# Performance work log

Measured on AMD Instinct MI355X. Metric: run time of the kernel, lower is better.

## Reference

```python
import jax, jax.numpy as jnp
import numpy as np

B, L, T, LM, DFF, D, H = 8, 256, 2048, 4096, 1024, 84, 4
HD = D // H  # 21
NCLS = 265


def _ln(x, s, b):
    m = x.mean(-1, keepdims=True)
    v = ((x - m) ** 2).mean(-1, keepdims=True)
    return (x - m) * jax.lax.rsqrt(v + 1e-5) * s + b


def _fourier(xyz, gB):
    # PositionEmbeddingCoordsSine(d_pos=10, pos_type='fourier'): xyz @ B * 2pi -> [sin, cos]
    proj = (2.0 * jnp.pi) * jnp.einsum('bnc,cd->bnd', xyz, gB)  # [B,N,5]
    return jnp.concatenate([jnp.sin(proj), jnp.cos(proj)], axis=-1)  # [B,N,10]


def setup_inputs() -> dict:
    key = jax.random.key(0)
    ks = jax.random.split(key, 20)
    def nrm(k, shape, scale):
        return jax.random.normal(k, shape, jnp.float32) * scale
    coords = jax.random.uniform(ks[0], (B, L, 6), jnp.float32)
    cls = jax.random.randint(ks[1], (B, L), 0, NCLS).astype(jnp.float32)
    vision_features = jnp.concatenate([coords, cls[..., None]], axis=-1)  # [B,L,7]
    FIN = D * L + LM  # 25600
    inp = {
        'grd_tokens': nrm(ks[2], (T, LM), 1.0),
        'vision_features': vision_features,
        'token_batch_idx': jax.random.randint(ks[3], (T,), 0, B),
        'gauss_B': nrm(ks[4], (3, 5), 1.0),
        'class_emb': nrm(ks[5], (NCLS, 64), 0.02),
        'w_in': nrm(ks[6], (2, D, 3 * D), D ** -0.5),
        'b_in': jnp.zeros((2, 3 * D), jnp.float32),
        'w_out': nrm(ks[7], (2, D, D), D ** -0.5),
        'b_out': jnp.zeros((2, D), jnp.float32),
        'ln1_s': jnp.ones((2, D), jnp.float32), 'ln1_b': jnp.zeros((2, D), jnp.float32),
        'w_ff1': nrm(ks[8], (2, D, DFF), D ** -0.5), 'b_ff1': jnp.zeros((2, DFF), jnp.float32),
        'w_ff2': nrm(ks[9], (2, DFF, D), DFF ** -0.5), 'b_ff2': jnp.zeros((2, D), jnp.float32),
        'ln2_s': jnp.ones((2, D), jnp.float32), 'ln2_b': jnp.zeros((2, D), jnp.float32),
        'w0': nrm(ks[10], (FIN, DFF), FIN ** -0.5), 'b0': jnp.zeros((DFF,), jnp.float32),
        'w1': nrm(ks[11], (DFF, DFF), DFF ** -0.5), 'b1': jnp.zeros((DFF,), jnp.float32),
        'w2': nrm(ks[12], (DFF, DFF), DFF ** -0.5), 'b2': jnp.zeros((DFF,), jnp.float32),
        'w3': nrm(ks[13], (DFF, DFF), DFF ** -0.5), 'b3': jnp.zeros((DFF,), jnp.float32),
        'w4': nrm(ks[14], (DFF, 6), DFF ** -0.5), 'b4': jnp.zeros((6,), jnp.float32),
    }
    return inp


def reference(grd_tokens, vision_features, token_batch_idx, gauss_B, class_emb,
              w_in, b_in, w_out, b_out, ln1_s, ln1_b, w_ff1, b_ff1, w_ff2, b_ff2,
              ln2_s, ln2_b, w0, b0, w1, b1, w2, b2, w3, b3, w4, b4):
    pe_min = _fourier(vision_features[:, :, 0:3], gauss_B)  # [B,L,10]
    pe_max = _fourier(vision_features[:, :, 3:6], gauss_B)  # [B,L,10]
    cls = vision_features[:, :, -1].astype(jnp.int32)
    src = jnp.concatenate([pe_min, pe_max, class_emb[cls]], axis=-1)  # [B,L,84]
    pad = jnp.all(vision_features == 0, axis=-1)  # [B,L]
    neg = jnp.where(pad, -1e9, 0.0)[:, None, None, :]  # [B,1,1,L] key-padding bias
    # 2-layer post-norm transformer encoder (DETR-style, pos=None, dropout=0)
    for l in range(2):
        qkv = src @ w_in[l] + b_in[l]
        q, k, v = jnp.split(qkv, 3, axis=-1)
        q = q.reshape(B, L, H, HD)
        k = k.reshape(B, L, H, HD)
        v = v.reshape(B, L, H, HD)
        scores = jnp.einsum('blhd,bmhd->bhlm', q, k) / jnp.sqrt(jnp.float32(HD)) + neg
        attn = jax.nn.softmax(scores, axis=-1)
        o = jnp.einsum('bhlm,bmhd->blhd', attn, v).reshape(B, L, D)
        src = _ln(src + o @ w_out[l] + b_out[l], ln1_s[l], ln1_b[l])
        ff = jax.nn.relu(src @ w_ff1[l] + b_ff1[l]) @ w_ff2[l] + b_ff2[l]
        src = _ln(src + ff, ln2_s[l], ln2_b[l])
    vision_flat = src.reshape(B, L * D)  # flattened encoder output per sample [B, 21504]
    # batched version of the ragged python loop: gather per-token vision feat + concat lm feat
    feat = jnp.concatenate([vision_flat[token_batch_idx], grd_tokens], axis=-1)  # [T, 25600]
    h = jax.nn.relu(feat @ w0 + b0)
    h = jax.nn.relu(h @ w1 + b1)
    h = jax.nn.relu(h @ w2 + b2)
    h = jax.nn.relu(h @ w3 + b3)
    return h @ w4 + b4  # [T, 6]
```

## Files before the change

### kernel.cpp

```cpp
#include <hip/hip_runtime.h>
#include <hip/hip_bf16.h>

#define B_ 8
#define L_ 256
#define T_ 2048
#define LM_ 4096
#define DFF_ 1024
#define D_ 84
#define H_ 4
#define HD_ 21
#define BL_ (B_*L_)
#define VISF_ (L_*D_)
#define VKS 168
#define VCHUNK (VISF_/VKS)
#define AKS 8
#define AKEYS (L_/AKS)

typedef __attribute__((ext_vector_type(8))) short bf16x8;
typedef __attribute__((ext_vector_type(4))) float f32x4;

typedef const __attribute__((address_space(1))) int* gas_p;
typedef __attribute__((address_space(3))) int* las_p;
__device__ __forceinline__ void gld_lds16(const void* g, void* l) {
    __builtin_amdgcn_global_load_lds((gas_p)g, (las_p)l, 16, 0, 0);
}

struct bh4 { __hip_bfloat16 x, y, z, w; };



__device__ __forceinline__ void dev_wT_pack(const float* __restrict__ W,
        __hip_bfloat16* __restrict__ Wp, int K, int N, int kb, int nb, int tid,
        float (*t)[33])
{
    int tx = tid & 31, ty = tid >> 5;
    #pragma unroll
    for (int i = 0; i < 4; ++i)
        t[ty + i*8][tx] = W[(size_t)(kb + ty + i*8)*N + nb + tx];
    __syncthreads();
    int KG = K >> 3;
    #pragma unroll
    for (int i = 0; i < 4; ++i) {
        int n = nb + ty + i*8, k = kb + tx;
        Wp[((size_t)(n>>4)*KG + (k>>3))*128 + (n&15)*8 + (k&7)] = __float2bfloat16(t[tx][ty + i*8]);
    }
}

__device__ __forceinline__ void dev_wTp_pack(const float* __restrict__ W,
        __hip_bfloat16* __restrict__ Wp, int K, int N, int KP, int kb, int nb, int tid,
        float (*t)[33])
{
    int tx = tid & 31, ty = tid >> 5;
    #pragma unroll
    for (int i = 0; i < 4; ++i) {
        int k = kb + ty + i*8, n = nb + tx;
        t[ty + i*8][tx] = (k < K && n < N) ? W[(size_t)k*N + n] : 0.0f;
    }
    __syncthreads();
    int KG = KP >> 3;
    #pragma unroll
    for (int i = 0; i < 4; ++i) {
        int n = nb + ty + i*8, k = kb + tx;
        Wp[((size_t)(n>>4)*KG + (k>>3))*128 + (n&15)*8 + (k&7)] = __float2bfloat16(t[tx][ty + i*8]);
    }
}

__device__ __forceinline__ void dev_wTp_row(const float* __restrict__ W,
        __hip_bfloat16* __restrict__ WT, int K, int N, int KP, int kb, int nb, int tid,
        float (*t)[33])
{
    int tx = tid & 31, ty = tid >> 5;
    #pragma unroll
    for (int i = 0; i < 4; ++i) {
        int k = kb + ty + i*8, n = nb + tx;
        t[ty + i*8][tx] = (k < K && n < N) ? W[(size_t)k*N + n] : 0.0f;
    }
    __syncthreads();
    #pragma unroll
    for (int i = 0; i < 4; ++i)
        WT[(size_t)(nb + ty + i*8)*KP + kb + tx] = __float2bfloat16(t[tx][ty + i*8]);
}

__device__ __forceinline__ void dev_f2b_pack(const float* __restrict__ in,
        __hip_bfloat16* __restrict__ out, int i)
{
    int row = i >> 9, kc = i & 511;
    const float4* p = reinterpret_cast<const float4*>(in + (size_t)row*4096 + kc*8);
    float4 v0 = p[0], v1 = p[1];
    bh4 a = { __float2bfloat16(v0.x), __float2bfloat16(v0.y),
              __float2bfloat16(v0.z), __float2bfloat16(v0.w) };
    bh4 b = { __float2bfloat16(v1.x), __float2bfloat16(v1.y),
              __float2bfloat16(v1.z), __float2bfloat16(v1.w) };
    __hip_bfloat16* o = out + ((size_t)(row>>4)*512 + kc)*128 + (row&15)*8;
    reinterpret_cast<bh4*>(o)[0] = a;
    reinterpret_cast<bh4*>(o)[1] = b;
}

__device__ __forceinline__ void dev_build_src(const float* __restrict__ vf,
        const float* __restrict__ gB, const float* __restrict__ cemb,
        float* __restrict__ src, float* __restrict__ neg, int row)
{
    float v[7];
    bool allz = true;
    #pragma unroll
    for (int c = 0; c < 7; ++c) { v[c] = vf[row*7 + c]; allz = allz && (v[c] == 0.0f); }
    neg[row] = allz ? -1e9f : 0.0f;
    float* s = src + (size_t)row * D_;
    const float TWO_PI = 6.28318530717958647692f;
    #pragma unroll
    for (int d = 0; d < 5; ++d) {
        float pmin = TWO_PI * (v[0]*gB[d] + v[1]*gB[5+d] + v[2]*gB[10+d]);
        float pmax = TWO_PI * (v[3]*gB[d] + v[4]*gB[5+d] + v[5]*gB[10+d]);
        s[d]      = sinf(pmin);  s[5+d]  = cosf(pmin);
        s[10+d]   = sinf(pmax);  s[15+d] = cosf(pmax);
    }
    int cls = (int)v[6];
    const float4* ce = reinterpret_cast<const float4*>(cemb + (size_t)cls*64);
    float4* so = reinterpret_cast<float4*>(s + 20);
    #pragma unroll
    for (int i = 0; i < 16; ++i) so[i] = ce[i];
}

__global__ __launch_bounds__(256) void k_pack_all(
        const float* __restrict__ grd, const float* __restrict__ w0,
        const float* __restrict__ w1, const float* __restrict__ w2,
        const float* __restrict__ w3, const float* __restrict__ w_ff1,
        const float* __restrict__ w_ff2,
        const float* __restrict__ vf, const float* __restrict__ gB,
        const float* __restrict__ cemb,
        __hip_bfloat16* __restrict__ grdb, __hip_bfloat16* __restrict__ w0t,
        __hip_bfloat16* __restrict__ w1t, __hip_bfloat16* __restrict__ w2t,
        __hip_bfloat16* __restrict__ w3t, __hip_bfloat16* __restrict__ wff1t,
        __hip_bfloat16* __restrict__ wff2t,
        float* __restrict__ src, float* __restrict__ neg)
{
    __shared__ float t[32][33];
    int blk = blockIdx.x, tid = threadIdx.x;
    if (blk < 4096) {
        dev_wT_pack(w0 + (size_t)VISF_*DFF_, w0t, LM_, DFF_,
                    (blk & 127)*32, (blk >> 7)*32, tid, t);
    } else if (blk < 5120) {
        int u = blk - 4096;
        dev_wT_pack(w1, w1t, DFF_, DFF_, (u & 31)*32, (u >> 5)*32, tid, t);
    } else if (blk < 6144) {
        int u = blk - 5120;
        dev_wT_pack(w2, w2t, DFF_, DFF_, (u & 31)*32, (u >> 5)*32, tid, t);
    } else if (blk < 7168) {
        int u = blk - 6144;
        dev_wT_pack(w3, w3t, DFF_, DFF_, (u & 31)*32, (u >> 5)*32, tid, t);
    } else if (blk < 7424) {
        int u = blk - 7168;
        int l = u >> 7; u &= 127;
        dev_wTp_pack(w_ff1 + (size_t)l*D_*DFF_, wff1t + (size_t)l*1024*128,
                     D_, DFF_, 128, (u & 3)*32, (u >> 2)*32, tid, t);
    } else if (blk < 7616) {
        int u = blk - 7424;
        int l = u / 96; u -= l*96;
        dev_wTp_row(w_ff2 + (size_t)l*DFF_*D_, wff2t + (size_t)l*96*1024,
                    DFF_, D_, 1024, (u % 32)*32, (u / 32)*32, tid, t);
    } else if (blk < 11712) {
        dev_f2b_pack(grd, grdb, (blk - 7616)*256 + tid);
    } else {
        dev_build_src(vf, gB, cemb, src, neg, (blk - 11712)*256 + tid);
    }
}

__global__ __launch_bounds__(256) void k_qkv8(const float* __restrict__ src,
        const float* __restrict__ w_in, const float* __restrict__ b_in,
        float* __restrict__ qkv, int lay)
{
    __shared__ float s8[8][D_];
    int r0 = blockIdx.x * 8, tid = threadIdx.x;
    for (int idx = tid; idx < 8*D_; idx += 256) {
        int r = idx / D_, d = idx - r*D_;
        s8[r][d] = src[(size_t)(r0+r)*D_ + d];
    }
    __syncthreads();
    if (tid < 3*D_) {
        const float* w = w_in + (size_t)lay*D_*3*D_ + tid;
        float acc[8] = {};
        for (int d = 0; d < D_; ++d) {
            float wv = w[(size_t)d*3*D_];
            #pragma unroll
            for (int r = 0; r < 8; ++r) acc[r] = fmaf(s8[r][d], wv, acc[r]);
        }
        float bv = b_in[lay*3*D_ + tid];
        #pragma unroll
        for (int r = 0; r < 8; ++r) qkv[(size_t)(r0+r)*(3*D_) + tid] = acc[r] + bv;
    }
}

__global__ __launch_bounds__(256) void k_attn_part(const float* __restrict__ qkv,
        const float* __restrict__ neg, float* __restrict__ part)
{
    __shared__ float ks_[AKEYS*HD_], vs_[AKEYS*HD_], ns[AKEYS];
    int bh = blockIdx.x;
    int b = bh >> 2, h = bh & 3;
    int sp = blockIdx.y;
    int tid = threadIdx.x;
    int k0 = sp * AKEYS;
    for (int idx = tid; idx < AKEYS*HD_; idx += 256) {
        int l = idx / HD_, d = idx - l*HD_;
        size_t base = ((size_t)(b*L_ + k0 + l))*(3*D_) + h*HD_ + d;
        ks_[idx] = qkv[base + D_];
        vs_[idx] = qkv[base + 2*D_];
    }
    if (tid < AKEYS) ns[tid] = neg[b*L_ + k0 + tid];
    __syncthreads();
    float q[HD_];
    {
        size_t base = ((size_t)(b*L_ + tid))*(3*D_) + h*HD_;
        #pragma unroll
        for (int d = 0; d < HD_; ++d) q[d] = qkv[base + d];
    }
    const float scale = 0.21821789023599239f;
    float m_run = -INFINITY, l_run = 0.0f;
    float o[HD_];
    #pragma unroll
    for (int d = 0; d < HD_; ++d) o[d] = 0.0f;
    for (int m = 0; m < AKEYS; ++m) {
        const float* krow = &ks_[m*HD_];
        float sdot = 0.0f;
        #pragma unroll
        for (int d = 0; d < HD_; ++d) sdot = fmaf(q[d], krow[d], sdot);
        float sc = sdot * scale + ns[m];
        float nm = fmaxf(m_run, sc);
        float c = __expf(m_run - nm);
        float p = __expf(sc - nm);
        l_run = l_run * c + p;
        const float* vrow = &vs_[m*HD_];
        #pragma unroll
        for (int d = 0; d < HD_; ++d) o[d] = fmaf(p, vrow[d], o[d]*c);
        m_run = nm;
    }
    float* po = part + (((size_t)bh*AKS + sp)*L_ + tid)*24;
    #pragma unroll
    for (int d = 0; d < HD_; ++d) po[d] = o[d];
    po[21] = m_run;
    po[22] = l_run;
}

__global__ __launch_bounds__(128) void k_oproj_ln(const float* __restrict__ part,
        const float* __restrict__ w_out, const float* __restrict__ b_out,
        const float* __restrict__ ln_s, const float* __restrict__ ln_b,
        float* __restrict__ src, __hip_bfloat16* __restrict__ srcb, int lay)
{
    __shared__ float os[D_];
    __shared__ float r1[128], r2[128];
    int row = blockIdx.x, tid = threadIdx.x;
    int b = row >> 8, q = row & 255;
    if (tid < D_) {
        int h = tid / 21, d = tid - h*21;
        const float* pb = part + (((size_t)(b*H_ + h)*AKS)*L_ + q)*24;
        float m_tot = -INFINITY;
        #pragma unroll
        for (int sp = 0; sp < AKS; ++sp)
            m_tot = fmaxf(m_tot, pb[(size_t)sp*L_*24 + 21]);
        float l_tot = 0.0f, ov = 0.0f;
        #pragma unroll
        for (int sp = 0; sp < AKS; ++sp) {
            const float* pp = pb + (size_t)sp*L_*24;
            float e = __expf(pp[21] - m_tot);
            l_tot = fmaf(pp[22], e, l_tot);
            ov = fmaf(pp[d], e, ov);
        }
        os[tid] = ov / l_tot;
    }
    __syncthreads();
    float y = 0.0f;
    if (tid < D_) {
        const float* w = w_out + (size_t)lay*D_*D_ + tid;
        float acc = b_out[lay*D_ + tid];
        for (int d = 0; d < D_; ++d) acc = fmaf(os[d], w[(size_t)d*D_], acc);
        y = src[(size_t)row*D_ + tid] + acc;
    }
    r1[tid] = (tid < D_) ? y : 0.0f;
    r2[tid] = (tid < D_) ? y*y : 0.0f;
    __syncthreads();
    for (int s = 64; s > 0; s >>= 1) {
        if (tid < s) { r1[tid] += r1[tid+s]; r2[tid] += r2[tid+s]; }
        __syncthreads();
    }
    float mean = r1[0] * (1.0f/D_);
    float var  = r2[0] * (1.0f/D_) - mean*mean;
    float rstd = rsqrtf(var + 1e-5f);
    float out = 0.0f;
    if (tid < D_) {
        out = (y - mean)*rstd*ln_s[lay*D_+tid] + ln_b[lay*D_+tid];
        src[(size_t)row*D_ + tid] = out;
    }
    __hip_bfloat16 val = (tid < D_) ? __float2bfloat16(out) : __float2bfloat16(0.0f);
    srcb[((size_t)(row>>4)*16 + (tid>>3))*128 + (row&15)*8 + (tid&7)] = val;
}

__global__ __launch_bounds__(256) void k_ff2_mfma(
        const __hip_bfloat16* __restrict__ hb,
        const __hip_bfloat16* __restrict__ wt,
        float* __restrict__ part)
{
    __shared__ __align__(16) __hip_bfloat16 sA[2][4096];
    __shared__ __align__(16) __hip_bfloat16 sB[2][6144];
    int tid = threadIdx.x;
    int bm = blockIdx.x * 64, sp = blockIdx.y;
    int wave = tid >> 6, lane = tid & 63;
    int wr = wave >> 1, wc = wave & 1;
    int l15 = lane & 15, l4 = lane >> 4;
    f32x4 acc[2][3] = {};

    const int row0 = bm + (tid & 63);
    const int kb = tid >> 6;
    const __hip_bfloat16* Ap0 = hb + (((size_t)(row0 >> 4)*128) + sp*16 + kb)*128 + (row0 & 15)*8;
    const __hip_bfloat16* Ap1 = Ap0 + 512;
    const int b_i0 = tid,       b_kb0 = b_i0/96, b_n0 = b_i0%96;
    const int b_i1 = tid + 256, b_kb1 = b_i1/96, b_n1 = b_i1%96;
    const int b_i2 = tid + 512, b_kb2 = b_i2/96, b_n2 = b_i2%96;
    const __hip_bfloat16* Bp0 = wt + (size_t)b_n0*1024 + sp*128 + b_kb0*8;
    const __hip_bfloat16* Bp1 = wt + (size_t)b_n1*1024 + sp*128 + b_kb1*8;
    const __hip_bfloat16* Bp2 = wt + (size_t)b_n2*1024 + sp*128 + b_kb2*8;

    gld_lds16(Ap0, (char*)&sA[0][0] + tid*16);
    gld_lds16(Ap1, (char*)&sA[0][0] + (tid+256)*16);
    gld_lds16(Bp0, (char*)&sB[0][0] + b_i0*16);
    gld_lds16(Bp1, (char*)&sB[0][0] + b_i1*16);
    gld_lds16(Bp2, (char*)&sB[0][0] + b_i2*16);
    #pragma unroll
    for (int t = 0; t < 2; ++t) {
        __syncthreads();
        if (t == 0) {
            gld_lds16(Ap0 + 1024, (char*)&sA[1][0] + tid*16);
            gld_lds16(Ap1 + 1024, (char*)&sA[1][0] + (tid+256)*16);
            gld_lds16(Bp0 + 64, (char*)&sB[1][0] + b_i0*16);
            gld_lds16(Bp1 + 64, (char*)&sB[1][0] + b_i1*16);
            gld_lds16(Bp2 + 64, (char*)&sB[1][0] + b_i2*16);
        }
        const __hip_bfloat16* sa = &sA[t][0];
        const __hip_bfloat16* sb = &sB[t][0];
        #pragma unroll
        for (int ks = 0; ks < 2; ++ks) {
            bf16x8 af[2], bfr[3];
            #pragma unroll
            for (int mi = 0; mi < 2; ++mi)
                af[mi] = *reinterpret_cast<const bf16x8*>(
                    &sa[(size_t)((ks*4 + l4)*64 + wr*32 + mi*16 + l15) * 8]);
            #pragma unroll
            for (int ni = 0; ni < 3; ++ni)
                bfr[ni] = *reinterpret_cast<const bf16x8*>(
                    &sb[(size_t)((ks*4 + l4)*96 + wc*48 + ni*16 + l15) * 8]);
            #pragma unroll
            for (int mi = 0; mi < 2; ++mi)
                #pragma unroll
                for (int ni = 0; ni < 3; ++ni)
                    acc[mi][ni] = __builtin_amdgcn_mfma_f32_16x16x32_bf16(
                        af[mi], bfr[ni], acc[mi][ni], 0, 0, 0);
        }
    }
    float* po = part + (size_t)sp*(2048*96);
    #pragma unroll
    for (int mi = 0; mi < 2; ++mi)
        #pragma unroll
        for (int reg = 0; reg < 4; ++reg) {
            int row = bm + wr*32 + mi*16 + l4*4 + reg;
            #pragma unroll
            for (int ni = 0; ni < 3; ++ni) {
                int col = wc*48 + ni*16 + l15;
                po[(size_t)row*96 + col] = acc[mi][ni][reg];
            }
        }
}

__global__ __launch_bounds__(128) void k_ff2ln_red(const float* __restrict__ part,
        const float* __restrict__ b_ff2, const float* __restrict__ ln_s,
        const float* __restrict__ ln_b, float* __restrict__ src, int lay)
{
    __shared__ float r1[128], r2[128];
    int row = blockIdx.x, tid = threadIdx.x;
    float y = 0.0f;
    if (tid < D_) {
        #pragma unroll
        for (int sp = 0; sp < 8; ++sp)
            y += part[(size_t)sp*(2048*96) + (size_t)row*96 + tid];
        y += b_ff2[lay*D_ + tid] + src[(size_t)row*D_ + tid];
    }
    r1[tid] = (tid < D_) ? y : 0.0f;
    r2[tid] = (tid < D_) ? y*y : 0.0f;
    __syncthreads();
    for (int s = 64; s > 0; s >>= 1) {
        if (tid < s) { r1[tid] += r1[tid+s]; r2[tid] += r2[tid+s]; }
        __syncthreads();
    }
    float mean = r1[0] * (1.0f/D_);
    float var  = r2[0] * (1.0f/D_) - mean*mean;
    float rstd = rsqrtf(var + 1e-5f);
    if (tid < D_)
        src[(size_t)row*D_ + tid] = (y - mean)*rstd*ln_s[lay*D_+tid] + ln_b[lay*D_+tid];
}

__global__ __launch_bounds__(256) void k_vis_gemm(const float* __restrict__ src,
        const float* __restrict__ w0, float* __restrict__ partials)
{
    __shared__ float vf[8][VCHUNK];
    __shared__ float red[8][256][4];
    int nt = blockIdx.x, sp = blockIdx.y, tid = threadIdx.x;
    int k0 = sp * VCHUNK;
    for (int idx = tid; idx < 8*VCHUNK; idx += 256) {
        int r = idx >> 7, c = idx & 127;
        vf[r][c] = src[(size_t)r*VISF_ + k0 + c];
    }
    __syncthreads();
    int ng = tid & 31;
    int kh = tid >> 5;
    const float* wp = w0 + (size_t)(k0 + kh*16)*DFF_ + nt*128 + ng*4;
    float acc[8][4] = {};
    #pragma unroll 4
    for (int kk = 0; kk < 16; ++kk) {
        float4 w = *reinterpret_cast<const float4*>(wp + (size_t)kk*DFF_);
        #pragma unroll
        for (int m = 0; m < 8; ++m) {
            float sv = vf[m][kh*16 + kk];
            acc[m][0] = fmaf(sv, w.x, acc[m][0]);
            acc[m][1] = fmaf(sv, w.y, acc[m][1]);
            acc[m][2] = fmaf(sv, w.z, acc[m][2]);
            acc[m][3] = fmaf(sv, w.w, acc[m][3]);
        }
    }
    #pragma unroll
    for (int m = 0; m < 8; ++m)
        *reinterpret_cast<float4*>(&red[m][tid][0]) =
            make_float4(acc[m][0], acc[m][1], acc[m][2], acc[m][3]);
    __syncthreads();
    int m2 = tid >> 5, ng2 = tid & 31;
    float4 s = *reinterpret_cast<const float4*>(&red[m2][ng2][0]);
    #pragma unroll
    for (int j = 1; j < 8; ++j) {
        float4 v = *reinterpret_cast<const float4*>(&red[m2][j*32 + ng2][0]);
        s.x += v.x; s.y += v.y; s.z += v.z; s.w += v.w;
    }
    *reinterpret_cast<float4*>(
        &partials[(size_t)sp*8192 + m2*1024 + nt*128 + ng2*4]) = s;
}

__global__ __launch_bounds__(256) void k_vis_red(const float* __restrict__ partials,
        float* __restrict__ vis)
{
    int o = blockIdx.x*256 + threadIdx.x;
    float s = 0.0f;
    for (int sp = 0; sp < VKS; ++sp) s += partials[(size_t)sp*8192 + o];
    vis[o] = s;
}

template<bool ADD_VIS, int K>
__global__ __launch_bounds__(256) void mfma_gemm(
        const __hip_bfloat16* __restrict__ Ap,
        const __hip_bfloat16* __restrict__ Bp,
        const float* __restrict__ bias,
        const float* __restrict__ vis,
        const int* __restrict__ bidx,
        __hip_bfloat16* __restrict__ Cp)
{
    constexpr int KG = K >> 3;
    constexpr int NG = 128;
    __shared__ __align__(16) __hip_bfloat16 cst[64*128];
    int tid = threadIdx.x, wave = tid >> 6, lane = tid & 63;
    int wr = wave >> 1, wc = wave & 1;
    int l15 = lane & 15, l4 = lane >> 4;
    int bm = blockIdx.x * 64, bn = blockIdx.y * 128;
    const __hip_bfloat16* Aw = Ap + ((size_t)((bm >> 4) + wr*2) * KG) * 128 + lane*8;
    const __hip_bfloat16* Bw = Bp + ((size_t)((bn >> 4) + wc*4) * KG) * 128 + lane*8;
    f32x4 acc[2][4] = {};

    #pragma unroll 4
    for (int kg = 0; kg < KG; kg += 4) {
        bf16x8 a[2], b[4];
        #pragma unroll
        for (int mi = 0; mi < 2; ++mi)
            a[mi] = *reinterpret_cast<const bf16x8*>(Aw + ((size_t)mi*KG + kg)*128);
        #pragma unroll
        for (int ni = 0; ni < 4; ++ni)
            b[ni] = *reinterpret_cast<const bf16x8*>(Bw + ((size_t)ni*KG + kg)*128);
        #pragma unroll
        for (int mi = 0; mi < 2; ++mi)
            #pragma unroll
            for (int ni = 0; ni < 4; ++ni)
                acc[mi][ni] = __builtin_amdgcn_mfma_f32_16x16x32_bf16(
                    a[mi], b[ni], acc[mi][ni], 0, 0, 0);
    }

    #pragma unroll
    for (int mi = 0; mi < 2; ++mi) {
        int mg = wr*2 + mi;
        #pragma unroll
        for (int ni = 0; ni < 4; ++ni) {
            int cg = wc*8 + ni*2 + (l15 >> 3);
            int c  = l15 & 7;
            int col = bn + cg*8 + c;
            float bv = bias[col];
            #pragma unroll
            for (int reg = 0; reg < 4; ++reg) {
                int r = l4*4 + reg;
                float v = acc[mi][ni][reg] + bv;
                if (ADD_VIS) v += vis[(size_t)bidx[bm + mg*16 + r]*1024 + col];
                v = fmaxf(v, 0.0f);
                cst[((mg*16 + cg)*16 + r)*8 + c] = __float2bfloat16(v);
            }
        }
    }
    __syncthreads();
    #pragma unroll
    for (int ch = tid; ch < 1024; ch += 256) {
        int mgcg = ch >> 4, r = ch & 15;
        int mg = mgcg >> 4, cg = mgcg & 15;
        size_t go = ((size_t)((bm >> 4) + mg) * NG + (bn >> 3) + cg) * 128 + r*8;
        *reinterpret_cast<bf16x8*>(Cp + go) =
            *reinterpret_cast<const bf16x8*>(cst + (size_t)ch*8);
    }
}

__global__ __launch_bounds__(64) void k_final(const __hip_bfloat16* __restrict__ hp,
        const float* __restrict__ w4, const float* __restrict__ b4, float* __restrict__ out)
{
    int t = blockIdx.x, lane = threadIdx.x;
    int mg = t >> 4, r = t & 15;
    float acc[6] = {};
    #pragma unroll
    for (int it = 0; it < 2; ++it) {
        int kg = lane + it*64;
        bf16x8 h = *reinterpret_cast<const bf16x8*>(hp + ((size_t)mg*128 + kg)*128 + r*8);
        #pragma unroll
        for (int j = 0; j < 8; ++j) {
            unsigned short us = (unsigned short)h[j];
            float hv = __uint_as_float((unsigned)us << 16);
            int k = kg*8 + j;
            #pragma unroll
            for (int c = 0; c < 6; ++c) acc[c] = fmaf(hv, w4[k*6 + c], acc[c]);
        }
    }
    #pragma unroll
    for (int j = 0; j < 6; ++j)
        #pragma unroll
        for (int s = 32; s > 0; s >>= 1) acc[j] += __shfl_down(acc[j], s);
    if (lane == 0) {
        #pragma unroll
        for (int j = 0; j < 6; ++j) out[(size_t)t*6 + j] = acc[j] + b4[j];
    }
}

extern "C" void kernel_launch(void* const* d_in, const int* in_sizes, int n_in,
                              void* d_out, int out_size, void* d_ws, size_t ws_size,
                              hipStream_t stream)
{
    const float* grd   = (const float*)d_in[0];
    const float* vfeat = (const float*)d_in[1];
    const int*   tbi   = (const int*)  d_in[2];
    const float* gB    = (const float*)d_in[3];
    const float* cemb  = (const float*)d_in[4];
    const float* w_in  = (const float*)d_in[5];
    const float* b_in  = (const float*)d_in[6];
    const float* w_out = (const float*)d_in[7];
    const float* b_out = (const float*)d_in[8];
    const float* ln1_s = (const float*)d_in[9];
    const float* ln1_b = (const float*)d_in[10];
    const float* w_ff1 = (const float*)d_in[11];
    const float* b_ff1 = (const float*)d_in[12];
    const float* w_ff2 = (const float*)d_in[13];
    const float* b_ff2 = (const float*)d_in[14];
    const float* ln2_s = (const float*)d_in[15];
    const float* ln2_b = (const float*)d_in[16];
    const float* w0    = (const float*)d_in[17];
    const float* b0    = (const float*)d_in[18];
    const float* w1    = (const float*)d_in[19];
    const float* b1    = (const float*)d_in[20];
    const float* w2    = (const float*)d_in[21];
    const float* b2    = (const float*)d_in[22];
    const float* w3    = (const float*)d_in[23];
    const float* b3    = (const float*)d_in[24];
    const float* w4    = (const float*)d_in[25];
    const float* b4    = (const float*)d_in[26];

    float* ws = (float*)d_ws;
    float* src    = ws;
    float* neg    = src    + 172032;
    float* qkv    = neg    + 2048;
    float* vparts = qkv    + 516096;
    float* visp   = vparts + 1376256;
    float* ffpart = visp   + 8192;
    float* fend   = ffpart + 1572864;
    __hip_bfloat16* grdb  = (__hip_bfloat16*)fend;
    __hip_bfloat16* w0t   = grdb  + 8388608;
    __hip_bfloat16* w1t   = w0t   + 4194304;
    __hip_bfloat16* w2t   = w1t   + 1048576;
    __hip_bfloat16* w3t   = w2t   + 1048576;
    __hip_bfloat16* hab   = w3t   + 1048576;
    __hip_bfloat16* hbb   = hab   + 2097152;
    __hip_bfloat16* srcb  = hbb   + 2097152;
    __hip_bfloat16* wff1t = srcb  + 262144;
    __hip_bfloat16* wff2t = wff1t + 262144;
    __hip_bfloat16* ffh   = hab;

    k_pack_all<<<11720, 256, 0, stream>>>(grd, w0, w1, w2, w3, w_ff1, w_ff2,
        vfeat, gB, cemb, grdb, w0t, w1t, w2t, w3t, wff1t, wff2t, src, neg);

    for (int lay = 0; lay < 2; ++lay) {
        k_qkv8     <<<BL_/8, 256, 0, stream>>>(src, w_in, b_in, qkv, lay);
        k_attn_part<<<dim3(B_*H_, AKS), 256, 0, stream>>>(qkv, neg, ffpart);
        k_oproj_ln <<<BL_, 128, 0, stream>>>(ffpart, w_out, b_out, ln1_s, ln1_b, src, srcb, lay);
        mfma_gemm<false, 128><<<dim3(32, 8), 256, 0, stream>>>(
            srcb, wff1t + (size_t)lay*1024*128, b_ff1 + lay*DFF_, nullptr, nullptr, ffh);
        k_ff2_mfma<<<dim3(32, 8), 256, 0, stream>>>(
            ffh, wff2t + (size_t)lay*96*1024, ffpart);
        k_ff2ln_red<<<BL_, 128, 0, stream>>>(ffpart, b_ff2, ln2_s, ln2_b, src, lay);
    }

    k_vis_gemm<<<dim3(8, VKS), 256, 0, stream>>>(src, w0, vparts);
    k_vis_red<<<32, 256, 0, stream>>>(vparts, visp);

    dim3 mg(T_/64, DFF_/128);
    mfma_gemm<true,  LM_ ><<<mg, 256, 0, stream>>>(grdb, w0t, b0, visp, tbi, hab);
    mfma_gemm<false, DFF_><<<mg, 256, 0, stream>>>(hab,  w1t, b1, nullptr, nullptr, hbb);
    mfma_gemm<false, DFF_><<<mg, 256, 0, stream>>>(hbb,  w2t, b2, nullptr, nullptr, hab);
    mfma_gemm<false, DFF_><<<mg, 256, 0, stream>>>(hab,  w3t, b3, nullptr, nullptr, hbb);

    k_final<<<T_, 64, 0, stream>>>(hbb, w4, b4, (float*)d_out);
}
```

Before: 240.6 us.

## Fuse QKV projection into attention kernel and read packed ff2 weights directly

```diff
diff --git a/kernel.cpp b/kernel.cpp
--- a/kernel.cpp
+++ b/kernel.cpp
@@ -19,14 +19,7 @@
 typedef __attribute__((ext_vector_type(8))) short bf16x8;
 typedef __attribute__((ext_vector_type(4))) float f32x4;
 
-typedef const __attribute__((address_space(1))) int* gas_p;
-typedef __attribute__((address_space(3))) int* las_p;
-__device__ __forceinline__ void gld_lds16(const void* g, void* l) {
-    __builtin_amdgcn_global_load_lds((gas_p)g, (las_p)l, 16, 0, 0);
-}
-
 struct bh4 { __hip_bfloat16 x, y, z, w; };
-
 
 
 __device__ __forceinline__ void dev_wT_pack(const float* __restrict__ W,
@@ -63,22 +56,6 @@
         int n = nb + ty + i*8, k = kb + tx;
         Wp[((size_t)(n>>4)*KG + (k>>3))*128 + (n&15)*8 + (k&7)] = __float2bfloat16(t[tx][ty + i*8]);
     }
-}
-
-__device__ __forceinline__ void dev_wTp_row(const float* __restrict__ W,
-        __hip_bfloat16* __restrict__ WT, int K, int N, int KP, int kb, int nb, int tid,
-        float (*t)[33])
-{
-    int tx = tid & 31, ty = tid >> 5;
-    #pragma unroll
-    for (int i = 0; i < 4; ++i) {
-        int k = kb + ty + i*8, n = nb + tx;
-        t[ty + i*8][tx] = (k < K && n < N) ? W[(size_t)k*N + n] : 0.0f;
-    }
-    __syncthreads();
-    #pragma unroll
-    for (int i = 0; i < 4; ++i)
-        WT[(size_t)(nb + ty + i*8)*KP + kb + tx] = __float2bfloat16(t[tx][ty + i*8]);
 }
 
 __device__ __forceinline__ void dev_f2b_pack(const float* __restrict__ in,
@@ -156,8 +133,8 @@
     } else if (blk < 7616) {
         int u = blk - 7424;
         int l = u / 96; u -= l*96;
-        dev_wTp_row(w_ff2 + (size_t)l*DFF_*D_, wff2t + (size_t)l*96*1024,
-                    DFF_, D_, 1024, (u % 32)*32, (u / 32)*32, tid, t);
+        dev_wTp_pack(w_ff2 + (size_t)l*DFF_*D_, wff2t + (size_t)l*98304,
+                     DFF_, D_, DFF_, (u % 32)*32, (u / 32)*32, tid, t);
     } else if (blk < 11712) {
         dev_f2b_pack(grd, grdb, (blk - 7616)*256 + tid);
     } else {
@@ -165,53 +142,50 @@
     }
 }
 
-__global__ __launch_bounds__(256) void k_qkv8(const float* __restrict__ src,
+__global__ __launch_bounds__(256) void k_attn_fused(const float* __restrict__ src,
         const float* __restrict__ w_in, const float* __restrict__ b_in,
-        float* __restrict__ qkv, int lay)
-{
-    __shared__ float s8[8][D_];
-    int r0 = blockIdx.x * 8, tid = threadIdx.x;
-    for (int idx = tid; idx < 8*D_; idx += 256) {
-        int r = idx / D_, d = idx - r*D_;
-        s8[r][d] = src[(size_t)(r0+r)*D_ + d];
-    }
-    __syncthreads();
-    if (tid < 3*D_) {
-        const float* w = w_in + (size_t)lay*D_*3*D_ + tid;
-        float acc[8] = {};
-        for (int d = 0; d < D_; ++d) {
-            float wv = w[(size_t)d*3*D_];
-            #pragma unroll
-            for (int r = 0; r < 8; ++r) acc[r] = fmaf(s8[r][d], wv, acc[r]);
+        const float* __restrict__ neg, float* __restrict__ part, int lay)
+{
+    __shared__ float ksrc[AKEYS][D_];
+    __shared__ float wq[D_][HD_], wk[D_][HD_], wv[D_][HD_];
+    __shared__ float ks_[AKEYS][HD_], vs_[AKEYS][HD_], ns[AKEYS];
+    int bh = blockIdx.x, b = bh >> 2, h = bh & 3;
+    int sp = blockIdx.y, tid = threadIdx.x;
+    int k0 = sp * AKEYS;
+    const float* wbase = w_in + (size_t)lay*D_*(3*D_);
+    for (int i = tid; i < D_*HD_; i += 256) {
+        int j = i / HD_, d = i - j*HD_;
+        const float* wr = wbase + (size_t)j*(3*D_) + h*HD_ + d;
+        wq[j][d] = wr[0];
+        wk[j][d] = wr[D_];
+        wv[j][d] = wr[2*D_];
+    }
+    for (int i = tid; i < AKEYS*D_; i += 256) {
+        int r = i / D_, c = i - r*D_;
+        ksrc[r][c] = src[(size_t)(b*L_ + k0 + r)*D_ + c];
+    }
+    if (tid < AKEYS) ns[tid] = neg[b*L_ + k0 + tid];
+    __syncthreads();
+    const float* bb = b_in + lay*(3*D_);
+    for (int i = tid; i < AKEYS*HD_; i += 256) {
+        int r = i / HD_, d = i - r*HD_;
+        float ak = bb[D_ + h*HD_ + d], av = bb[2*D_ + h*HD_ + d];
+        for (int j = 0; j < D_; ++j) {
+            float s = ksrc[r][j];
+            ak = fmaf(s, wk[j][d], ak);
+            av = fmaf(s, wv[j][d], av);
         }
-        float bv = b_in[lay*3*D_ + tid];
-        #pragma unroll
-        for (int r = 0; r < 8; ++r) qkv[(size_t)(r0+r)*(3*D_) + tid] = acc[r] + bv;
-    }
-}
-
-__global__ __launch_bounds__(256) void k_attn_part(const float* __restrict__ qkv,
-        const float* __restrict__ neg, float* __restrict__ part)
-{
-    __shared__ float ks_[AKEYS*HD_], vs_[AKEYS*HD_], ns[AKEYS];
-    int bh = blockIdx.x;
-    int b = bh >> 2, h = bh & 3;
-    int sp = blockIdx.y;
-    int tid = threadIdx.x;
-    int k0 = sp * AKEYS;
-    for (int idx = tid; idx < AKEYS*HD_; idx += 256) {
-        int l = idx / HD_, d = idx - l*HD_;
-        size_t base = ((size_t)(b*L_ + k0 + l))*(3*D_) + h*HD_ + d;
-        ks_[idx] = qkv[base + D_];
-        vs_[idx] = qkv[base + 2*D_];
-    }
-    if (tid < AKEYS) ns[tid] = neg[b*L_ + k0 + tid];
+        ks_[r][d] = ak; vs_[r][d] = av;
+    }
     __syncthreads();
     float q[HD_];
-    {
-        size_t base = ((size_t)(b*L_ + tid))*(3*D_) + h*HD_;
-        #pragma unroll
-        for (int d = 0; d < HD_; ++d) q[d] = qkv[base + d];
+    #pragma unroll
+    for (int d = 0; d < HD_; ++d) q[d] = bb[h*HD_ + d];
+    const float* srow = src + (size_t)(b*L_ + tid)*D_;
+    for (int j = 0; j < D_; ++j) {
+        float s = srow[j];
+        #pragma unroll
+        for (int d = 0; d < HD_; ++d) q[d] = fmaf(s, wq[j][d], q[d]);
     }
     const float scale = 0.21821789023599239f;
     float m_run = -INFINITY, l_run = 0.0f;
@@ -219,18 +193,16 @@
     #pragma unroll
     for (int d = 0; d < HD_; ++d) o[d] = 0.0f;
     for (int m = 0; m < AKEYS; ++m) {
-        const float* krow = &ks_[m*HD_];
         float sdot = 0.0f;
         #pragma unroll
-        for (int d = 0; d < HD_; ++d) sdot = fmaf(q[d], krow[d], sdot);
+        for (int d = 0; d < HD_; ++d) sdot = fmaf(q[d], ks_[m][d], sdot);
         float sc = sdot * scale + ns[m];
         float nm = fmaxf(m_run, sc);
         float c = __expf(m_run - nm);
         float p = __expf(sc - nm);
         l_run = l_run * c + p;
-        const float* vrow = &vs_[m*HD_];
-        #pragma unroll
-        for (int d = 0; d < HD_; ++d) o[d] = fmaf(p, vrow[d], o[d]*c);
+        #pragma unroll
+        for (int d = 0; d < HD_; ++d) o[d] = fmaf(p, vs_[m][d], o[d]*c);
         m_run = nm;
     }
     float* po = part + (((size_t)bh*AKS + sp)*L_ + tid)*24;
@@ -295,64 +267,33 @@
 
 __global__ __launch_bounds__(256) void k_ff2_mfma(
         const __hip_bfloat16* __restrict__ hb,
-        const __hip_bfloat16* __restrict__ wt,
+        const __hip_bfloat16* __restrict__ wp,
         float* __restrict__ part)
 {
-    __shared__ __align__(16) __hip_bfloat16 sA[2][4096];
-    __shared__ __align__(16) __hip_bfloat16 sB[2][6144];
-    int tid = threadIdx.x;
-    int bm = blockIdx.x * 64, sp = blockIdx.y;
-    int wave = tid >> 6, lane = tid & 63;
+    int tid = threadIdx.x, wave = tid >> 6, lane = tid & 63;
     int wr = wave >> 1, wc = wave & 1;
     int l15 = lane & 15, l4 = lane >> 4;
+    int bm = blockIdx.x * 64, sp = blockIdx.y;
+    const __hip_bfloat16* Aw = hb + ((size_t)((bm >> 4) + wr*2) * 128) * 128 + lane*8;
+    const __hip_bfloat16* Bw = wp + ((size_t)(wc*3) * 128) * 128 + lane*8;
     f32x4 acc[2][3] = {};
-
-    const int row0 = bm + (tid & 63);
-    const int kb = tid >> 6;
-    const __hip_bfloat16* Ap0 = hb + (((size_t)(row0 >> 4)*128) + sp*16 + kb)*128 + (row0 & 15)*8;
-    const __hip_bfloat16* Ap1 = Ap0 + 512;
-    const int b_i0 = tid,       b_kb0 = b_i0/96, b_n0 = b_i0%96;
-    const int b_i1 = tid + 256, b_kb1 = b_i1/96, b_n1 = b_i1%96;
-    const int b_i2 = tid + 512, b_kb2 = b_i2/96, b_n2 = b_i2%96;
-    const __hip_bfloat16* Bp0 = wt + (size_t)b_n0*1024 + sp*128 + b_kb0*8;
-    const __hip_bfloat16* Bp1 = wt + (size_t)b_n1*1024 + sp*128 + b_kb1*8;
-    const __hip_bfloat16* Bp2 = wt + (size_t)b_n2*1024 + sp*128 + b_kb2*8;
-
-    gld_lds16(Ap0, (char*)&sA[0][0] + tid*16);
-    gld_lds16(Ap1, (char*)&sA[0][0] + (tid+256)*16);
-    gld_lds16(Bp0, (char*)&sB[0][0] + b_i0*16);
-    gld_lds16(Bp1, (char*)&sB[0][0] + b_i1*16);
-    gld_lds16(Bp2, (char*)&sB[0][0] + b_i2*16);
-    #pragma unroll
-    for (int t = 0; t < 2; ++t) {
-        __syncthreads();
-        if (t == 0) {
-            gld_lds16(Ap0 + 1024, (char*)&sA[1][0] + tid*16);
-            gld_lds16(Ap1 + 1024, (char*)&sA[1][0] + (tid+256)*16);
-            gld_lds16(Bp0 + 64, (char*)&sB[1][0] + b_i0*16);
-            gld_lds16(Bp1 + 64, (char*)&sB[1][0] + b_i1*16);
-            gld_lds16(Bp2 + 64, (char*)&sB[1][0] + b_i2*16);
-        }
-        const __hip_bfloat16* sa = &sA[t][0];
-        const __hip_bfloat16* sb = &sB[t][0];
-        #pragma unroll
-        for (int ks = 0; ks < 2; ++ks) {
-            bf16x8 af[2], bfr[3];
-            #pragma unroll
-            for (int mi = 0; mi < 2; ++mi)
-                af[mi] = *reinterpret_cast<const bf16x8*>(
-                    &sa[(size_t)((ks*4 + l4)*64 + wr*32 + mi*16 + l15) * 8]);
+    int kg0 = sp * 16;
+    #pragma unroll
+    for (int kk = 0; kk < 16; kk += 4) {
+        int kg = kg0 + kk;
+        bf16x8 a[2], b[3];
+        #pragma unroll
+        for (int mi = 0; mi < 2; ++mi)
+            a[mi] = *reinterpret_cast<const bf16x8*>(Aw + ((size_t)mi*128 + kg)*128);
+        #pragma unroll
+        for (int ni = 0; ni < 3; ++ni)
+            b[ni] = *reinterpret_cast<const bf16x8*>(Bw + ((size_t)ni*128 + kg)*128);
+        #pragma unroll
+        for (int mi = 0; mi < 2; ++mi)
             #pragma unroll
             for (int ni = 0; ni < 3; ++ni)
-                bfr[ni] = *reinterpret_cast<const bf16x8*>(
-                    &sb[(size_t)((ks*4 + l4)*96 + wc*48 + ni*16 + l15) * 8]);
-            #pragma unroll
-            for (int mi = 0; mi < 2; ++mi)
-                #pragma unroll
-                for (int ni = 0; ni < 3; ++ni)
-                    acc[mi][ni] = __builtin_amdgcn_mfma_f32_16x16x32_bf16(
-                        af[mi], bfr[ni], acc[mi][ni], 0, 0, 0);
-        }
+                acc[mi][ni] = __builtin_amdgcn_mfma_f32_16x16x32_bf16(
+                    a[mi], b[ni], acc[mi][ni], 0, 0, 0);
     }
     float* po = part + (size_t)sp*(2048*96);
     #pragma unroll
@@ -579,8 +520,7 @@
     float* ws = (float*)d_ws;
     float* src    = ws;
     float* neg    = src    + 172032;
-    float* qkv    = neg    + 2048;
-    float* vparts = qkv    + 516096;
+    float* vparts = neg    + 2048;
     float* visp   = vparts + 1376256;
     float* ffpart = visp   + 8192;
     float* fend   = ffpart + 1572864;
@@ -600,13 +540,12 @@
         vfeat, gB, cemb, grdb, w0t, w1t, w2t, w3t, wff1t, wff2t, src, neg);
 
     for (int lay = 0; lay < 2; ++lay) {
-        k_qkv8     <<<BL_/8, 256, 0, stream>>>(src, w_in, b_in, qkv, lay);
-        k_attn_part<<<dim3(B_*H_, AKS), 256, 0, stream>>>(qkv, neg, ffpart);
-        k_oproj_ln <<<BL_, 128, 0, stream>>>(ffpart, w_out, b_out, ln1_s, ln1_b, src, srcb, lay);
+        k_attn_fused<<<dim3(B_*H_, AKS), 256, 0, stream>>>(src, w_in, b_in, neg, ffpart, lay);
+        k_oproj_ln  <<<BL_, 128, 0, stream>>>(ffpart, w_out, b_out, ln1_s, ln1_b, src, srcb, lay);
         mfma_gemm<false, 128><<<dim3(32, 8), 256, 0, stream>>>(
             srcb, wff1t + (size_t)lay*1024*128, b_ff1 + lay*DFF_, nullptr, nullptr, ffh);
         k_ff2_mfma<<<dim3(32, 8), 256, 0, stream>>>(
-            ffh, wff2t + (size_t)lay*96*1024, ffpart);
+            ffh, wff2t + (size_t)lay*98304, ffpart);
         k_ff2ln_red<<<BL_, 128, 0, stream>>>(ffpart, b_ff2, ln2_s, ln2_b, src, lay);
     }
 
```

Measured after the change: 252.2 us. +4.8%, slower.
